# Performance work log

Hardware: AMD Instinct MI355X
Metric: run time of the kernel (lower is better)

Reference implementation:

```python
import jax, jax.numpy as jnp
import numpy as np

B, T, C = 2, 2048, 1024
NH = 16

def setup_inputs() -> dict:
    key = jax.random.key(0)
    ks = jax.random.split(key, 5)
    s = 0.02
    return {
        "x": jax.random.normal(ks[0], (B, T, C), dtype=jnp.float32),
        "w_attn": jax.random.normal(ks[1], (C, 3 * C), dtype=jnp.float32) * s,
        "b_attn": jax.random.normal(ks[2], (3 * C,), dtype=jnp.float32) * s,
        "w_proj": jax.random.normal(ks[3], (C, C), dtype=jnp.float32) * s,
        "b_proj": jax.random.normal(ks[4], (C,), dtype=jnp.float32) * s,
        "n_heads": NH,
    }

def reference(x, w_attn, b_attn, w_proj, b_proj, n_heads):
    Bx, Tx, Cx = x.shape
    hd = Cx // n_heads
    qkv = x @ w_attn + b_attn                      # [B,T,3C]
    q, k, v = jnp.split(qkv, 3, axis=-1)
    # [B,T,H,hd] -> [B,H,T,hd]
    q = q.reshape(Bx, Tx, n_heads, hd).transpose(0, 2, 1, 3)
    k = k.reshape(Bx, Tx, n_heads, hd).transpose(0, 2, 1, 3)
    v = v.reshape(Bx, Tx, n_heads, hd).transpose(0, 2, 1, 3)
    scale = 1.0 / np.sqrt(hd).astype(np.float32)
    att = jnp.einsum('bhqd,bhkd->bhqk', q, k) * scale   # [B,H,T,T]
    causal = jnp.tril(jnp.ones((Tx, Tx), dtype=bool))
    att = jnp.where(causal[None, None], att, -jnp.inf)
    att = jax.nn.softmax(att, axis=-1)
    y = jnp.einsum('bhqk,bhkd->bhqd', att, v)            # [B,H,T,hd]
    y = y.transpose(0, 2, 1, 3).reshape(Bx, Tx, Cx)
    return y @ w_proj + b_proj
```

## Files before the change

### kernel.cpp

```cpp
#include <hip/hip_runtime.h>

typedef __bf16 bf16x8 __attribute__((ext_vector_type(8)));
typedef __bf16 bf16x4 __attribute__((ext_vector_type(4)));
typedef float  f32x4  __attribute__((ext_vector_type(4)));
typedef float  f32x16 __attribute__((ext_vector_type(16)));
typedef unsigned int u32;

#define MFMA_BF16(a, b, c) __builtin_amdgcn_mfma_f32_16x16x32_bf16((a), (b), (c), 0, 0, 0)
#define MFMA32(a, b, c) __builtin_amdgcn_mfma_f32_32x32x16_bf16((a), (b), (c), 0, 0, 0)
#define NEG_INF (-1e30f)
#define SCL 0.18033688f

__device__ __forceinline__ void gld16(const void* g, void* l) {
  __builtin_amdgcn_global_load_lds(
      (const __attribute__((address_space(1))) void*)g,
      (__attribute__((address_space(3))) void*)l, 16, 0, 0);
}

__global__ void cast_f32_bf16(const float* __restrict__ in,
                              __bf16* __restrict__ out, int n) {
  int i = (blockIdx.x * 256 + threadIdx.x) * 8;
  if (i >= n) return;
  float4 a = *(const float4*)&in[i];
  float4 b = *(const float4*)&in[i + 4];
  bf16x8 v;
  v[0] = (__bf16)a.x; v[1] = (__bf16)a.y; v[2] = (__bf16)a.z; v[3] = (__bf16)a.w;
  v[4] = (__bf16)b.x; v[5] = (__bf16)b.y; v[6] = (__bf16)b.z; v[7] = (__bf16)b.w;
  *(bf16x8*)&out[i] = v;
}

__global__ void transpose_f32_bf16(const float* __restrict__ in,
                                   __bf16* __restrict__ out, int R, int C) {
  __shared__ float t[32][33];
  int tx = threadIdx.x & 31, ty = threadIdx.x >> 5;
  int x = blockIdx.x * 32 + tx;
  int y0 = blockIdx.y * 32 + ty;
#pragma unroll
  for (int i = 0; i < 4; ++i)
    t[ty + 8 * i][tx] = in[(size_t)(y0 + 8 * i) * C + x];
  __syncthreads();
  int x2 = blockIdx.y * 32 + tx;
#pragma unroll
  for (int i = 0; i < 4; ++i)
    out[(size_t)(blockIdx.x * 32 + ty + 8 * i) * R + x2] = (__bf16)t[tx][ty + 8 * i];
}

#define BN 128
#define BK 64

template <int BMT, typename TC>
__global__ __launch_bounds__(256) void gemm_bt_bias(
    const __bf16* __restrict__ A, const __bf16* __restrict__ Bt,
    const float* __restrict__ bias, TC* __restrict__ Cmat,
    int M, int N, int K) {
  constexpr int NI = BMT / 32;
  __shared__ __align__(16) __bf16 As[BMT * BK];
  __shared__ __align__(16) __bf16 Bs[BN * BK];
  int tid = threadIdx.x;
  int wave = tid >> 6, lane = tid & 63;
  int l16 = lane & 15, quad = lane >> 4;
  int wm = wave >> 1, wn = wave & 1;
  int m0 = blockIdx.y * BMT, n0 = blockIdx.x * BN;

  f32x4 acc[NI][4];
#pragma unroll
  for (int i = 0; i < NI; ++i)
#pragma unroll
    for (int j = 0; j < 4; ++j) acc[i][j] = (f32x4){0.f, 0.f, 0.f, 0.f};

  int row = tid >> 3;
  int kc = ((tid & 7) ^ ((tid >> 3) & 7)) * 8;
  int xr = (l16 & 7) * 8;

  for (int k0 = 0; k0 < K; k0 += BK) {
#pragma unroll
    for (int i = 0; i < NI; ++i)
      gld16(&A[(size_t)(m0 + row + i * 32) * K + k0 + kc],
            (char*)As + (i * 256 + wave * 64) * 16);
#pragma unroll
    for (int j = 0; j < 4; ++j)
      gld16(&Bt[(size_t)(n0 + row + j * 32) * K + k0 + kc],
            (char*)Bs + (j * 256 + wave * 64) * 16);
    __syncthreads();
#pragma unroll
    for (int ks = 0; ks < 2; ++ks) {
      bf16x8 af[NI], bfr[4];
#pragma unroll
      for (int i = 0; i < NI; ++i)
        af[i] = *(const bf16x8*)&As[(wm * (BMT / 2) + i * 16 + l16) * BK +
                                    ((ks * 32 + quad * 8) ^ xr)];
#pragma unroll
      for (int j = 0; j < 4; ++j)
        bfr[j] = *(const bf16x8*)&Bs[(wn * 64 + j * 16 + l16) * BK +
                                     ((ks * 32 + quad * 8) ^ xr)];
#pragma unroll
      for (int i = 0; i < NI; ++i)
#pragma unroll
        for (int j = 0; j < 4; ++j) acc[i][j] = MFMA_BF16(af[i], bfr[j], acc[i][j]);
    }
    __syncthreads();
  }
#pragma unroll
  for (int i = 0; i < NI; ++i) {
#pragma unroll
    for (int j = 0; j < 4; ++j) {
      int col = n0 + wn * 64 + j * 16 + l16;
      float bv = bias[col];
#pragma unroll
      for (int r = 0; r < 4; ++r) {
        int rw = m0 + wm * (BMT / 2) + i * 16 + quad * 4 + r;
        Cmat[(size_t)rw * N + col] = (TC)(acc[i][j][r] + bv);
      }
    }
  }
}

#define BARX do { asm volatile("" ::: "memory"); __builtin_amdgcn_s_barrier(); \
                  asm volatile("" ::: "memory"); } while (0)
#define WLGKM do { asm volatile("s_waitcnt lgkmcnt(0)" ::: "memory"); \
                   __builtin_amdgcn_sched_barrier(0); } while (0)
#define WVM4 asm volatile("s_waitcnt vmcnt(4)" ::: "memory")
#define STA8(SBUF, SKS, T) do { \
    gld16(srcA1 + (size_t)(T) * 64 + (SKS) * 32, (char*)&As[SBUF][SKS][0] + tid * 16); \
    gld16(srcA2 + (size_t)(T) * 64 + (SKS) * 32, (char*)&As[SBUF][SKS][0] + tid * 16 + 8192); \
  } while (0)
#define STB8(SBUF, SKS, T) do { \
    gld16(srcB1 + (size_t)(T) * 64 + (SKS) * 32, (char*)&Bs[SBUF][SKS][0] + tid * 16); \
    gld16(srcB2 + (size_t)(T) * 64 + (SKS) * 32, (char*)&Bs[SBUF][SKS][0] + tid * 16 + 8192); \
  } while (0)
#define LDA4(CBUF, CKS, MQ) do { \
    const __bf16* p_ = &As[CBUF][CKS][(wm * 128 + (MQ) * 64 + l16) * 32 + xrd]; \
    af[0] = *(const bf16x8*)(p_);        af[1] = *(const bf16x8*)(p_ + 512); \
    af[2] = *(const bf16x8*)(p_ + 1024); af[3] = *(const bf16x8*)(p_ + 1536); \
  } while (0)
#define LDB3(CBUF, CKS) do { \
    const __bf16* p_ = &Bs[CBUF][CKS][(wn * 48 + l16) * 32 + xrd]; \
    bfr[0] = *(const bf16x8*)(p_);       bfr[1] = *(const bf16x8*)(p_ + 512); \
    bfr[2] = *(const bf16x8*)(p_ + 1024); \
  } while (0)
#define MM12(MQ) do { \
    __builtin_amdgcn_s_setprio(1); \
    _Pragma("unroll") for (int mi_ = 0; mi_ < 4; ++mi_) \
    _Pragma("unroll") for (int nj_ = 0; nj_ < 3; ++nj_) \
      acc[(MQ) * 4 + mi_][nj_] = MFMA_BF16(af[mi_], bfr[nj_], acc[(MQ) * 4 + mi_][nj_]); \
    __builtin_amdgcn_s_setprio(0); \
  } while (0)

__global__ __launch_bounds__(512, 2) void gemm_qkv_8ph(
    const __bf16* __restrict__ A, const __bf16* __restrict__ Bt,
    const float* __restrict__ bias, __bf16* __restrict__ qkv,
    __bf16* __restrict__ vt) {
  constexpr int GK = 1024, GN = 3072, NT = 16;
  __shared__ __align__(16) __bf16 As[2][2][256 * 32];
  __shared__ __align__(16) __bf16 Bs[2][2][256 * 32];
  const int tid = threadIdx.x;
  const int wave = tid >> 6, lane = tid & 63;
  const int l16 = lane & 15, quad = lane >> 4;
  const int wm = wave >> 2, wn = wave & 3;
  const int m0 = blockIdx.y * 256, n0 = blockIdx.x * 192;

  const int row0 = tid >> 2;
  const int kc = (((tid & 3) ^ ((row0 >> 1) & 3)) * 8);
  const int xrd = (quad ^ ((l16 >> 1) & 3)) * 8;

  const __bf16* srcA1 = A + (size_t)(m0 + row0) * GK + kc;
  const __bf16* srcA2 = srcA1 + (size_t)128 * GK;
  const __bf16* srcB1 = Bt + (size_t)(n0 + row0) * GK + kc;
  const int br2 = (row0 + 128 < 192) ? row0 + 128 : 191;
  const __bf16* srcB2 = Bt + (size_t)(n0 + br2) * GK + kc;

  f32x4 acc[8][3];
#pragma unroll
  for (int m = 0; m < 8; ++m)
#pragma unroll
    for (int n = 0; n < 3; ++n) acc[m][n] = (f32x4){0.f, 0.f, 0.f, 0.f};

  STA8(0, 0, 0); STB8(0, 0, 0);
  STA8(0, 1, 0); STB8(0, 1, 0);
  STA8(1, 0, 1); STB8(1, 0, 1);
  WVM4;
  BARX;

  bf16x8 af[4], bfr[3];
#pragma unroll 1
  for (int i = 0; i < NT / 2; ++i) {
    const int v = 2 * i + 1;
    const int t2 = (2 * i + 2 < NT) ? 2 * i + 2 : NT - 1;
    const int t3 = (2 * i + 3 < NT) ? 2 * i + 3 : NT - 1;
    LDA4(0, 0, 0); LDB3(0, 0); STA8(1, 1, v);
    BARX; WLGKM; MM12(0); BARX;
    LDA4(0, 0, 1); STB8(1, 1, v);
    BARX; WLGKM; MM12(1); BARX;
    LDA4(0, 1, 0); LDB3(0, 1); STA8(0, 0, t2);
    BARX; WLGKM; MM12(0); BARX;
    LDA4(0, 1, 1); STB8(0, 0, t2);
    BARX; WLGKM; MM12(1); WVM4; BARX;
    LDA4(1, 0, 0); LDB3(1, 0); STA8(0, 1, t2);
    BARX; WLGKM; MM12(0); BARX;
    LDA4(1, 0, 1); STB8(0, 1, t2);
    BARX; WLGKM; MM12(1); BARX;
    LDA4(1, 1, 0); LDB3(1, 1); STA8(1, 0, t3);
    BARX; WLGKM; MM12(0); BARX;
    LDA4(1, 1, 1); STB8(1, 0, t3);
    BARX; WLGKM; MM12(1); WVM4; BARX;
  }

#pragma unroll
  for (int n = 0; n < 3; ++n) {
    const int c0 = n0 + wn * 48 + n * 16;
    const int col = c0 + l16;
    const float bv = bias[col];
    if (c0 < 2048) {
#pragma unroll
      for (int m = 0; m < 8; ++m) {
        const int rw = m0 + wm * 128 + m * 16 + quad * 4;
#pragma unroll
        for (int r = 0; r < 4; ++r)
          qkv[(size_t)(rw + r) * GN + col] = (__bf16)(acc[m][n][r] + bv);
      }
    } else {
      const int h = (col - 2048) >> 6, d = col & 63;
#pragma unroll
      for (int m = 0; m < 8; ++m) {
        const int t0 = m0 + wm * 128 + m * 16 + quad * 4;
        const int b = t0 >> 11, tt = t0 & 2047;
        bf16x4 pb;
#pragma unroll
        for (int r = 0; r < 4; ++r) pb[r] = (__bf16)(acc[m][n][r] + bv);
        *(bf16x4*)&vt[(size_t)((b * 16 + h) * 64 + d) * 2048 + tt] = pb;
      }
    }
  }
}

#define CVTPK(D, LO, HI) \
  asm("v_cvt_pk_bf16_f32 %0, %1, %2" : "=v"(D) : "v"(LO), "v"(HI))
#define SWAP32(DST, SRC) \
  asm("v_permlane32_swap_b32 %0, %1" : "+v"(DST), "+v"(SRC))

__device__ __forceinline__ bf16x8 mk8(u32 a, u32 b, u32 c, u32 d) {
  union { u32 u[4]; bf16x8 h; } x;
  x.u[0] = a; x.u[1] = b; x.u[2] = c; x.u[3] = d;
  return x.h;
}

__global__ __launch_bounds__(512, 4) void attn_causal(
    const __bf16* __restrict__ qkv, const __bf16* __restrict__ vt,
    __bf16* __restrict__ y) {
  __shared__ __align__(16) __bf16 smem[2][2][2][64 * 64];
  const int tid = threadIdx.x;
  const int wave = tid >> 6, lane = tid & 63;
  const int l32 = lane & 31, hi = lane >> 5;
  const int qh = wave >> 1, kh = wave & 1;
  const int bh = blockIdx.x;
  const int b = bh >> 4, h = bh & 15;
  const int RS = 3072;
  const int by = (int)blockIdx.y;
  const int qb = (by < 8) ? 15 - by : by - 8;
  const int nit = qb + 1;
  const int ktmax = 2 * qb + (qh >> 1);

  const int row8 = tid >> 3;
  const int kcs = (((tid & 7) ^ (row8 & 7) ^ ((row8 >> 3) & 3)) * 8);
  const __bf16* kbase = qkv + (size_t)(b * 2048) * RS + 1024 + h * 64 + kcs;
  const __bf16* vbase = vt + (size_t)(bh * 64) * 2048 + kcs;
  const int xr = (l32 & 7) ^ ((l32 >> 3) & 3);

  const __bf16* qp = qkv +
      (size_t)(b * 2048 + qb * 128 + qh * 32 + l32) * RS + h * 64 + hi * 8;
  bf16x8 qf[4];
#pragma unroll
  for (int kc = 0; kc < 4; ++kc) qf[kc] = *(const bf16x8*)(qp + kc * 16);

  float l4[4] = {0.f, 0.f, 0.f, 0.f};
  f32x16 o0, o1;
#pragma unroll
  for (int r = 0; r < 16; ++r) { o0[r] = 0.f; o1[r] = 0.f; }

#pragma unroll
  for (int s = 0; s < 2; ++s) {
    gld16(kbase + (size_t)(s * 64 + row8) * RS, (char*)smem[0][0][s] + tid * 16);
    gld16(vbase + (size_t)row8 * 2048 + s * 64, (char*)smem[1][0][s] + tid * 16);
  }
  __syncthreads();

  for (int it = 0; it < nit; ++it) {
    const int cur = it & 1;
    if (it < qb) {
      const int kb2 = (it + 1) * 128;
#pragma unroll
      for (int s = 0; s < 2; ++s) {
        gld16(kbase + (size_t)(kb2 + s * 64 + row8) * RS,
              (char*)smem[0][cur ^ 1][s] + tid * 16);
        gld16(vbase + (size_t)row8 * 2048 + kb2 + s * 64,
              (char*)smem[1][cur ^ 1][s] + tid * 16);
      }
    }

    const int kt = 2 * it + kh;
    if (kt <= ktmax) {
      const __bf16* Kc = smem[0][cur][kh];
      const __bf16* Vc = smem[1][cur][kh];

      f32x16 c0, c1;
#pragma unroll
      for (int r = 0; r < 16; ++r) { c0[r] = 0.f; c1[r] = 0.f; }
      __builtin_amdgcn_s_setprio(1);
#pragma unroll
      for (int kc = 0; kc < 4; ++kc) {
        const int sw = ((kc * 2 + hi) ^ xr) << 3;
        bf16x8 kf0 = *(const bf16x8*)&Kc[l32 * 64 + sw];
        bf16x8 kf1 = *(const bf16x8*)&Kc[(32 + l32) * 64 + sw];
        c0 = MFMA32(kf0, qf[kc], c0);
        c1 = MFMA32(kf1, qf[kc], c1);
      }
      __builtin_amdgcn_s_setprio(0);

      if (kt == ktmax) {
        const int qloc = qh * 32 + l32 - (kt - 2 * qb) * 64;
#pragma unroll
        for (int r = 0; r < 16; ++r) {
          const int kl = (r & 3) + 8 * (r >> 2) + 4 * hi;
          if (kl > qloc) c0[r] = NEG_INF;
          if (32 + kl > qloc) c1[r] = NEG_INF;
        }
      }

      bf16x8 pb[4];
#pragma unroll
      for (int kb = 0; kb < 2; ++kb) {
        float pv[16];
#pragma unroll
        for (int r = 0; r < 16; ++r) {
          const float sv = (kb ? c1[r] : c0[r]);
          pv[r] = __builtin_amdgcn_exp2f(sv * SCL);
          l4[r & 3] += pv[r];
        }
        u32 a0, a1, b0, b1;
        CVTPK(a0, pv[0], pv[1]);   CVTPK(a1, pv[2], pv[3]);
        CVTPK(b0, pv[4], pv[5]);   CVTPK(b1, pv[6], pv[7]);
        SWAP32(a0, b0); SWAP32(a1, b1);
        pb[kb * 2 + 0] = mk8(a0, a1, b0, b1);
        CVTPK(a0, pv[8], pv[9]);   CVTPK(a1, pv[10], pv[11]);
        CVTPK(b0, pv[12], pv[13]); CVTPK(b1, pv[14], pv[15]);
        SWAP32(a0, b0); SWAP32(a1, b1);
        pb[kb * 2 + 1] = mk8(a0, a1, b0, b1);

        __builtin_amdgcn_s_setprio(1);
#pragma unroll
        for (int kq = 0; kq < 2; ++kq) {
          const int kc = kb * 2 + kq;
          const int sw = ((kc * 2 + hi) ^ xr) << 3;
          bf16x8 vf0 = *(const bf16x8*)&Vc[l32 * 64 + sw];
          bf16x8 vf1 = *(const bf16x8*)&Vc[(32 + l32) * 64 + sw];
          o0 = MFMA32(vf0, pb[kc], o0);
          o1 = MFMA32(vf1, pb[kc], o1);
        }
        __builtin_amdgcn_s_setprio(0);
      }
    }
    __syncthreads();
  }

  float lred = (l4[0] + l4[1]) + (l4[2] + l4[3]);
  lred += __shfl_xor(lred, 32);

  float* sc = (float*)smem;
  if (kh == 1) {
    float* ob = sc + qh * 2048;
#pragma unroll
    for (int r = 0; r < 16; ++r) {
      ob[r * 64 + lane] = o0[r];
      ob[1024 + r * 64 + lane] = o1[r];
    }
    if (lane < 32) sc[8192 + qh * 32 + lane] = lred;
  }
  __syncthreads();
  if (kh == 0) {
    const float* ob = sc + qh * 2048;
    lred += sc[8192 + qh * 32 + l32];
    const float inv = 1.f / lred;
    const int orow = b * 2048 + qb * 128 + qh * 32 + l32;
    __bf16* yb = y + (size_t)orow * 1024 + h * 64 + hi * 4;
#pragma unroll
    for (int db = 0; db < 2; ++db) {
#pragma unroll
      for (int g = 0; g < 4; ++g) {
        bf16x4 w;
#pragma unroll
        for (int j = 0; j < 4; ++j) {
          const float v = (db ? o1[g * 4 + j] : o0[g * 4 + j]) +
                          ob[db * 1024 + (g * 4 + j) * 64 + lane];
          w[j] = (__bf16)(v * inv);
        }
        *(bf16x4*)&yb[db * 32 + g * 8] = w;
      }
    }
  }
}

extern "C" void kernel_launch(void* const* d_in, const int* in_sizes, int n_in,
                              void* d_out, int out_size, void* d_ws, size_t ws_size,
                              hipStream_t stream) {
  (void)in_sizes; (void)n_in; (void)out_size; (void)ws_size;
  const float* x      = (const float*)d_in[0];
  const float* w_attn = (const float*)d_in[1];
  const float* b_attn = (const float*)d_in[2];
  const float* w_proj = (const float*)d_in[3];
  const float* b_proj = (const float*)d_in[4];
  float* out = (float*)d_out;

  __bf16* wt_attn = (__bf16*)d_ws;
  __bf16* wt_proj = wt_attn + (size_t)3072 * 1024;
  __bf16* qkv     = wt_proj + (size_t)1024 * 1024;
  __bf16* ybuf    = qkv + (size_t)4096 * 3072;
  __bf16* vtbuf   = ybuf + (size_t)4096 * 1024;

  cast_f32_bf16<<<4096 * 1024 / 2048, 256, 0, stream>>>(x, ybuf, 4096 * 1024);

  transpose_f32_bf16<<<dim3(3072 / 32, 1024 / 32), 256, 0, stream>>>(w_attn, wt_attn, 1024, 3072);
  transpose_f32_bf16<<<dim3(1024 / 32, 1024 / 32), 256, 0, stream>>>(w_proj, wt_proj, 1024, 1024);

  gemm_qkv_8ph<<<dim3(3072 / 192, 4096 / 256), 512, 0, stream>>>(
      ybuf, wt_attn, b_attn, qkv, vtbuf);

  attn_causal<<<dim3(32, 16), 512, 0, stream>>>(qkv, vtbuf, ybuf);

  gemm_bt_bias<64, float><<<dim3(1024 / BN, 4096 / 64), 256, 0, stream>>>(
      ybuf, wt_proj, b_proj, out, 4096, 1024, 1024);
}
```

Baseline: 169.2 us.

## Merge prep kernels into one launch and restructure QKV GEMM phases

Replaces the cast kernel and the two weight-transpose launches with a single prep kernel that dispatches on block index, removing two kernel launches. The QKV GEMM main loop moves from 8 half-tile phases to 4 full-tile phases: each phase loads all 8 A fragments and issues 24 MFMAs, and both A and B stage loads are issued together with a vmcnt(8) wait. This halves the number of barriers and waits per K step, at the cost of more live A-fragment registers, which could hurt occupancy at launch_bounds(512,2).

```diff
diff --git a/kernel.cpp b/kernel.cpp
--- a/kernel.cpp
+++ b/kernel.cpp
@@ -17,32 +17,38 @@
       (__attribute__((address_space(3))) void*)l, 16, 0, 0);
 }
 
-__global__ void cast_f32_bf16(const float* __restrict__ in,
-                              __bf16* __restrict__ out, int n) {
-  int i = (blockIdx.x * 256 + threadIdx.x) * 8;
-  if (i >= n) return;
-  float4 a = *(const float4*)&in[i];
-  float4 b = *(const float4*)&in[i + 4];
-  bf16x8 v;
-  v[0] = (__bf16)a.x; v[1] = (__bf16)a.y; v[2] = (__bf16)a.z; v[3] = (__bf16)a.w;
-  v[4] = (__bf16)b.x; v[5] = (__bf16)b.y; v[6] = (__bf16)b.z; v[7] = (__bf16)b.w;
-  *(bf16x8*)&out[i] = v;
-}
-
-__global__ void transpose_f32_bf16(const float* __restrict__ in,
-                                   __bf16* __restrict__ out, int R, int C) {
+__global__ __launch_bounds__(256) void prep(
+    const float* __restrict__ x, __bf16* __restrict__ xb,
+    const float* __restrict__ wa, __bf16* __restrict__ wta,
+    const float* __restrict__ wp, __bf16* __restrict__ wtp) {
   __shared__ float t[32][33];
-  int tx = threadIdx.x & 31, ty = threadIdx.x >> 5;
-  int x = blockIdx.x * 32 + tx;
-  int y0 = blockIdx.y * 32 + ty;
+  const int tid = threadIdx.x;
+  const int bx = blockIdx.x;
+  if (bx < 2048) {
+    int i = (bx * 256 + tid) * 8;
+    float4 a = *(const float4*)&x[i];
+    float4 b = *(const float4*)&x[i + 4];
+    bf16x8 v;
+    v[0] = (__bf16)a.x; v[1] = (__bf16)a.y; v[2] = (__bf16)a.z; v[3] = (__bf16)a.w;
+    v[4] = (__bf16)b.x; v[5] = (__bf16)b.y; v[6] = (__bf16)b.z; v[7] = (__bf16)b.w;
+    *(bf16x8*)&xb[i] = v;
+    return;
+  }
+  const float* in; __bf16* out; int R, C, bxx, byy;
+  if (bx < 5120) { in = wa; out = wta; R = 1024; C = 3072;
+                   bxx = (bx - 2048) % 96; byy = (bx - 2048) / 96; }
+  else           { in = wp; out = wtp; R = 1024; C = 1024;
+                   bxx = (bx - 5120) % 32; byy = (bx - 5120) / 32; }
+  int tx = tid & 31, ty = tid >> 5;
+  int xx = bxx * 32 + tx, y0 = byy * 32 + ty;
 #pragma unroll
   for (int i = 0; i < 4; ++i)
-    t[ty + 8 * i][tx] = in[(size_t)(y0 + 8 * i) * C + x];
+    t[ty + 8 * i][tx] = in[(size_t)(y0 + 8 * i) * C + xx];
   __syncthreads();
-  int x2 = blockIdx.y * 32 + tx;
+  int x2 = byy * 32 + tx;
 #pragma unroll
   for (int i = 0; i < 4; ++i)
-    out[(size_t)(blockIdx.x * 32 + ty + 8 * i) * R + x2] = (__bf16)t[tx][ty + 8 * i];
+    out[(size_t)(bxx * 32 + ty + 8 * i) * R + x2] = (__bf16)t[tx][ty + 8 * i];
 }
 
 #define BN 128
@@ -119,7 +125,7 @@
                   asm volatile("" ::: "memory"); } while (0)
 #define WLGKM do { asm volatile("s_waitcnt lgkmcnt(0)" ::: "memory"); \
                    __builtin_amdgcn_sched_barrier(0); } while (0)
-#define WVM4 asm volatile("s_waitcnt vmcnt(4)" ::: "memory")
+#define WVM8 asm volatile("s_waitcnt vmcnt(8)" ::: "memory")
 #define STA8(SBUF, SKS, T) do { \
     gld16(srcA1 + (size_t)(T) * 64 + (SKS) * 32, (char*)&As[SBUF][SKS][0] + tid * 16); \
     gld16(srcA2 + (size_t)(T) * 64 + (SKS) * 32, (char*)&As[SBUF][SKS][0] + tid * 16 + 8192); \
@@ -128,21 +134,24 @@
     gld16(srcB1 + (size_t)(T) * 64 + (SKS) * 32, (char*)&Bs[SBUF][SKS][0] + tid * 16); \
     gld16(srcB2 + (size_t)(T) * 64 + (SKS) * 32, (char*)&Bs[SBUF][SKS][0] + tid * 16 + 8192); \
   } while (0)
-#define LDA4(CBUF, CKS, MQ) do { \
-    const __bf16* p_ = &As[CBUF][CKS][(wm * 128 + (MQ) * 64 + l16) * 32 + xrd]; \
-    af[0] = *(const bf16x8*)(p_);        af[1] = *(const bf16x8*)(p_ + 512); \
-    af[2] = *(const bf16x8*)(p_ + 1024); af[3] = *(const bf16x8*)(p_ + 1536); \
+#define LDA8(CBUF, CKS) do { \
+    const __bf16* p0_ = &As[CBUF][CKS][(wm * 128 + l16) * 32 + xrd]; \
+    af[0] = *(const bf16x8*)(p0_);        af[1] = *(const bf16x8*)(p0_ + 512); \
+    af[2] = *(const bf16x8*)(p0_ + 1024); af[3] = *(const bf16x8*)(p0_ + 1536); \
+    const __bf16* p1_ = p0_ + 2048; \
+    af[4] = *(const bf16x8*)(p1_);        af[5] = *(const bf16x8*)(p1_ + 512); \
+    af[6] = *(const bf16x8*)(p1_ + 1024); af[7] = *(const bf16x8*)(p1_ + 1536); \
   } while (0)
 #define LDB3(CBUF, CKS) do { \
     const __bf16* p_ = &Bs[CBUF][CKS][(wn * 48 + l16) * 32 + xrd]; \
     bfr[0] = *(const bf16x8*)(p_);       bfr[1] = *(const bf16x8*)(p_ + 512); \
     bfr[2] = *(const bf16x8*)(p_ + 1024); \
   } while (0)
-#define MM12(MQ) do { \
+#define MM24 do { \
     __builtin_amdgcn_s_setprio(1); \
-    _Pragma("unroll") for (int mi_ = 0; mi_ < 4; ++mi_) \
+    _Pragma("unroll") for (int mi_ = 0; mi_ < 8; ++mi_) \
     _Pragma("unroll") for (int nj_ = 0; nj_ < 3; ++nj_) \
-      acc[(MQ) * 4 + mi_][nj_] = MFMA_BF16(af[mi_], bfr[nj_], acc[(MQ) * 4 + mi_][nj_]); \
+      acc[mi_][nj_] = MFMA_BF16(af[mi_], bfr[nj_], acc[mi_][nj_]); \
     __builtin_amdgcn_s_setprio(0); \
   } while (0)
 
@@ -178,31 +187,23 @@
   STA8(0, 0, 0); STB8(0, 0, 0);
   STA8(0, 1, 0); STB8(0, 1, 0);
   STA8(1, 0, 1); STB8(1, 0, 1);
-  WVM4;
+  WVM8;
   BARX;
 
-  bf16x8 af[4], bfr[3];
+  bf16x8 af[8], bfr[3];
 #pragma unroll 1
   for (int i = 0; i < NT / 2; ++i) {
     const int v = 2 * i + 1;
     const int t2 = (2 * i + 2 < NT) ? 2 * i + 2 : NT - 1;
     const int t3 = (2 * i + 3 < NT) ? 2 * i + 3 : NT - 1;
-    LDA4(0, 0, 0); LDB3(0, 0); STA8(1, 1, v);
-    BARX; WLGKM; MM12(0); BARX;
-    LDA4(0, 0, 1); STB8(1, 1, v);
-    BARX; WLGKM; MM12(1); BARX;
-    LDA4(0, 1, 0); LDB3(0, 1); STA8(0, 0, t2);
-    BARX; WLGKM; MM12(0); BARX;
-    LDA4(0, 1, 1); STB8(0, 0, t2);
-    BARX; WLGKM; MM12(1); WVM4; BARX;
-    LDA4(1, 0, 0); LDB3(1, 0); STA8(0, 1, t2);
-    BARX; WLGKM; MM12(0); BARX;
-    LDA4(1, 0, 1); STB8(0, 1, t2);
-    BARX; WLGKM; MM12(1); BARX;
-    LDA4(1, 1, 0); LDB3(1, 1); STA8(1, 0, t3);
-    BARX; WLGKM; MM12(0); BARX;
-    LDA4(1, 1, 1); STB8(1, 0, t3);
-    BARX; WLGKM; MM12(1); WVM4; BARX;
+    LDA8(0, 0); LDB3(0, 0); STA8(1, 1, v); STB8(1, 1, v);
+    BARX; WLGKM; MM24; WVM8; BARX;
+    LDA8(0, 1); LDB3(0, 1); STA8(0, 0, t2); STB8(0, 0, t2);
+    BARX; WLGKM; MM24; WVM8; BARX;
+    LDA8(1, 0); LDB3(1, 0); STA8(0, 1, t2); STB8(0, 1, t2);
+    BARX; WLGKM; MM24; WVM8; BARX;
+    LDA8(1, 1); LDB3(1, 1); STA8(1, 0, t3); STB8(1, 0, t3);
+    BARX; WLGKM; MM24; WVM8; BARX;
   }
 
 #pragma unroll
@@ -416,10 +417,7 @@
   __bf16* ybuf    = qkv + (size_t)4096 * 3072;
   __bf16* vtbuf   = ybuf + (size_t)4096 * 1024;
 
-  cast_f32_bf16<<<4096 * 1024 / 2048, 256, 0, stream>>>(x, ybuf, 4096 * 1024);
-
-  transpose_f32_bf16<<<dim3(3072 / 32, 1024 / 32), 256, 0, stream>>>(w_attn, wt_attn, 1024, 3072);
-  transpose_f32_bf16<<<dim3(1024 / 32, 1024 / 32), 256, 0, stream>>>(w_proj, wt_proj, 1024, 1024);
+  prep<<<6144, 256, 0, stream>>>(x, ybuf, w_attn, wt_attn, w_proj, wt_proj);
 
   gemm_qkv_8ph<<<dim3(3072 / 192, 4096 / 256), 512, 0, stream>>>(
       ybuf, wt_attn, b_attn, qkv, vtbuf);
```

Result: no change. 170.6 us (+0.8%).
